# Kernel tuning notes

Measured on AMD Instinct MI355X. Metric: run time of the kernel, lower is better.

The kernel has to match this reference:

```python
import jax, jax.numpy as jnp
import numpy as np

EMBED_DIM = 768
NUM_HEADS = 12
HEAD_DIM = EMBED_DIM // NUM_HEADS  # 64
B, N = 2, 3073
SCALE = HEAD_DIM ** -0.5


def setup_inputs() -> dict:
    key = jax.random.key(0)
    ks = jax.random.split(key, 6)
    s = EMBED_DIM ** -0.5
    return {
        "x": jax.random.normal(ks[0], (B, N, EMBED_DIM), dtype=jnp.float32),
        "qkv_w": jax.random.normal(ks[1], (3 * EMBED_DIM, EMBED_DIM), dtype=jnp.float32) * s,
        "proj_w": jax.random.normal(ks[2], (EMBED_DIM, EMBED_DIM), dtype=jnp.float32) * s,
        "proj_b": jax.random.normal(ks[3], (EMBED_DIM,), dtype=jnp.float32) * 0.02,
        "conv_w": jax.random.normal(ks[4], (HEAD_DIM, 1, 3, 3), dtype=jnp.float32) * 0.02,
        "conv_b": jax.random.normal(ks[5], (HEAD_DIM,), dtype=jnp.float32) * 0.02,
    }


def _local_pos_embed(v, conv_w, conv_b):
    # v: [B, H, N, C] with C = head_dim; drop cls token, fold to spatial grid
    b, h, n, c = v.shape
    u = int(((n - 1) // 12) ** 0.5)
    Hh, Ww = 4 * u, 3 * u
    xs = jnp.transpose(v[:, :, 1:], (0, 1, 3, 2)).reshape(b * h, c, Hh, Ww)
    pe = jax.lax.conv_general_dilated(
        xs, conv_w, window_strides=(1, 1), padding=((1, 1), (1, 1)),
        feature_group_count=c, dimension_numbers=("NCHW", "OIHW", "NCHW"))
    pe = pe + conv_b[None, :, None, None]
    pe = pe.reshape(b, h, c, n - 1).transpose(0, 1, 3, 2)  # [B,H,N-1,C]
    zeros = jnp.zeros((b, h, 1, c), dtype=pe.dtype)
    return jnp.concatenate([zeros, pe], axis=2)  # [B,H,N,C]


def reference(x, qkv_w, proj_w, proj_b, conv_w, conv_b):
    b, n, d = x.shape
    qkv = x @ qkv_w.T  # [B, N, 3D]
    qkv = qkv.reshape(b, n, 3, NUM_HEADS, HEAD_DIM).transpose(2, 0, 3, 1, 4)  # [3,B,H,N,Dh]
    q, k, v = qkv[0], qkv[1], qkv[2]
    scores = jnp.einsum("bhqd,bhkd->bhqk", q, k) * SCALE
    attn = jax.nn.softmax(scores, axis=-1)
    out = jnp.einsum("bham,bhmv->bhav", attn, v)  # [B,H,N,Dh]
    out = out + _local_pos_embed(v, conv_w, conv_b)
    out = out.transpose(0, 2, 1, 3).reshape(b, n, d)  # b h n d -> b n (h d)
    return out @ proj_w.T + proj_b
```

## Files before the change

kernel.cpp:

```cpp
#include <hip/hip_runtime.h>
#include <math.h>

#define NB 2
#define SEQ 3073
#define DIM 768
#define NH 12
#define DH 64
#define HHH 64
#define WWW 48
#define NPATCH 3072
#define QSCALE_L2E 0.18033688f
#define KSPLIT 1536

#define BHN (NB * NH)
#define MROWS (NB * SEQ)
#define MPAD 6272
#define CNT (BHN * SEQ * DH)
#define VTSTRIDE 3136

typedef __attribute__((ext_vector_type(8))) short s8v;
typedef __attribute__((ext_vector_type(4))) float f4v;
typedef __attribute__((ext_vector_type(4))) ushort u4v;

#define MFMA16(a, b, c) __builtin_amdgcn_mfma_f32_16x16x32_bf16((a), (b), (c), 0, 0, 0)

__device__ __forceinline__ ushort f2bf(float f) {
    unsigned x = __float_as_uint(f);
    return (ushort)((x + 0x7FFFu + ((x >> 16) & 1u)) >> 16);
}
__device__ __forceinline__ float bf2f(ushort u) {
    return __uint_as_float(((unsigned)u) << 16);
}
__device__ __forceinline__ unsigned cvt_pk_bf16(float a, float b) {
    unsigned r;
    asm("v_cvt_pk_bf16_f32 %0, %1, %2" : "=v"(r) : "v"(a), "v"(b));
    return r;
}

__device__ __forceinline__ s8v ldsFrag(const ushort* base, int row, int half, int t) {
    int byte = (row * 128 + half * 64 + t * 16) ^ ((row & 7) << 4);
    return *(const s8v*)((const char*)base + byte);
}

__global__ __launch_bounds__(256) void cast_bf16(const float* __restrict__ in,
                                                 ushort* __restrict__ out,
                                                 int n_in, int n_grp) {
    for (int g = blockIdx.x * 256 + threadIdx.x; g < n_grp; g += gridDim.x * 256) {
        int i0 = g * 4;
        float4 vv;
        if (i0 + 4 <= n_in) {
            vv = *(const float4*)(in + i0);
        } else {
            vv.x = (i0 + 0 < n_in) ? in[i0 + 0] : 0.f;
            vv.y = (i0 + 1 < n_in) ? in[i0 + 1] : 0.f;
            vv.z = (i0 + 2 < n_in) ? in[i0 + 2] : 0.f;
            vv.w = (i0 + 3 < n_in) ? in[i0 + 3] : 0.f;
        }
        u4v hv;
        hv[0] = f2bf(vv.x); hv[1] = f2bf(vv.y);
        hv[2] = f2bf(vv.z); hv[3] = f2bf(vv.w);
        *(u4v*)(out + i0) = hv;
    }
}

__global__ __launch_bounds__(256) void split_hilo(const float* __restrict__ in,
                                                  ushort* __restrict__ hi,
                                                  ushort* __restrict__ lo,
                                                  int n_in, int n_grp) {
    for (int g = blockIdx.x * 256 + threadIdx.x; g < n_grp; g += gridDim.x * 256) {
        int i0 = g * 4;
        float4 vv = *(const float4*)(in + i0);
        float v[4] = {vv.x, vv.y, vv.z, vv.w};
        u4v hv, lv;
        #pragma unroll
        for (int j = 0; j < 4; ++j) {
            ushort hb = f2bf(v[j]);
            hv[j] = hb;
            lv[j] = f2bf(v[j] - bf2f(hb));
        }
        *(u4v*)(hi + i0) = hv;
        *(u4v*)(lo + i0) = lv;
    }
}

__device__ __forceinline__ void mfma_tile_768_a1(const ushort* __restrict__ gA,
                                                 const ushort* __restrict__ gBh,
                                                 const ushort* __restrict__ gBl,
                                                 ushort* Ah, ushort* Bh, ushort* Bl,
                                                 f4v acc[4][4]) {
    const int tid = threadIdx.x;
    const int lane = tid & 63;
    const int w = tid >> 6;
    const int lo = lane & 15, t = lane >> 4;
    const int wr = w >> 1, wc = w & 1;

    for (int k0 = 0; k0 < DIM; k0 += 64) {
        __syncthreads();
        #pragma unroll
        for (int i = 0; i < 4; ++i) {
            int s = tid + 256 * i;
            int r = s >> 3, c = s & 7;
            int byte = (r * 128 + c * 16) ^ ((r & 7) << 4);
            size_t go = (size_t)r * DIM + k0 + c * 8;
            s8v a0 = *(const s8v*)(gA + go);
            s8v b0 = *(const s8v*)(gBh + go);
            s8v b1 = *(const s8v*)(gBl + go);
            *(s8v*)((char*)Ah + byte) = a0;
            *(s8v*)((char*)Bh + byte) = b0;
            *(s8v*)((char*)Bl + byte) = b1;
        }
        __syncthreads();

        #pragma unroll
        for (int h = 0; h < 2; ++h) {
            s8v af[4];
            #pragma unroll
            for (int i = 0; i < 4; ++i)
                af[i] = ldsFrag(Ah, wr * 64 + i * 16 + lo, h, t);
            #pragma unroll
            for (int j = 0; j < 4; ++j) {
                int row = wc * 64 + j * 16 + lo;
                s8v bf_h = ldsFrag(Bh, row, h, t);
                s8v bf_l = ldsFrag(Bl, row, h, t);
                #pragma unroll
                for (int i = 0; i < 4; ++i) {
                    acc[i][j] = MFMA16(af[i], bf_h, acc[i][j]);
                    acc[i][j] = MFMA16(af[i], bf_l, acc[i][j]);
                }
            }
        }
    }
}

__global__ __launch_bounds__(256) void qkv_mfma(const ushort* __restrict__ xh,
                                                const ushort* __restrict__ wh,
                                                const ushort* __restrict__ wl,
                                                ushort* __restrict__ q_bf,
                                                ushort* __restrict__ k_bf,
                                                ushort* __restrict__ v_bf,
                                                ushort* __restrict__ vt) {
    __shared__ ushort Ah[8192], Bh[8192], Bl[8192];
    const int m0 = blockIdx.x * 128;
    const int nb = blockIdx.y;
    f4v acc[4][4] = {};
    mfma_tile_768_a1(xh + (size_t)m0 * DIM,
                     wh + (size_t)nb * 128 * DIM, wl + (size_t)nb * 128 * DIM,
                     Ah, Bh, Bl, acc);

    const int tid = threadIdx.x;
    const int lane = tid & 63;
    const int w = tid >> 6;
    const int lo = lane & 15, t = lane >> 4;
    const int wr = w >> 1, wc = w & 1;
    const int which = nb / 6;
    const int rr0 = (nb % 6) * 128;

    #pragma unroll
    for (int i = 0; i < 4; ++i) {
        #pragma unroll
        for (int r = 0; r < 4; ++r) {
            int m = m0 + wr * 64 + i * 16 + t * 4 + r;
            if (m >= MROWS) continue;
            int bb = m / SEQ;
            int row = m - bb * SEQ;
            #pragma unroll
            for (int j = 0; j < 4; ++j) {
                int rr = rr0 + wc * 64 + j * 16 + lo;
                int hh = rr >> 6, dd = rr & 63;
                size_t base = ((size_t)(bb * NH + hh) * SEQ + row) * DH + dd;
                float val = acc[i][j][r];
                if (which == 0) {
                    q_bf[base] = f2bf(val * QSCALE_L2E);
                } else if (which == 1) {
                    k_bf[base] = f2bf(val);
                } else {
                    ushort vb = f2bf(val);
                    v_bf[base] = vb;
                    vt[((size_t)(bb * NH + hh) * DH + dd) * VTSTRIDE + row] = vb;
                }
            }
        }
    }
}

__global__ __launch_bounds__(256) void proj_mfma(const ushort* __restrict__ ah,
                                                 const ushort* __restrict__ pwh,
                                                 const ushort* __restrict__ pwl,
                                                 const float* __restrict__ bias,
                                                 float* __restrict__ out) {
    __shared__ ushort Ah[8192], Bh[8192], Bl[8192];
    const int m0 = blockIdx.x * 128;
    const int nb = blockIdx.y;
    f4v acc[4][4] = {};
    mfma_tile_768_a1(ah + (size_t)m0 * DIM,
                     pwh + (size_t)nb * 128 * DIM, pwl + (size_t)nb * 128 * DIM,
                     Ah, Bh, Bl, acc);

    const int tid = threadIdx.x;
    const int lane = tid & 63;
    const int w = tid >> 6;
    const int lo = lane & 15, t = lane >> 4;
    const int wr = w >> 1, wc = w & 1;

    #pragma unroll
    for (int i = 0; i < 4; ++i) {
        #pragma unroll
        for (int r = 0; r < 4; ++r) {
            int m = m0 + wr * 64 + i * 16 + t * 4 + r;
            if (m >= MROWS) continue;
            #pragma unroll
            for (int j = 0; j < 4; ++j) {
                int n = nb * 128 + wc * 64 + j * 16 + lo;
                out[(size_t)m * DIM + n] = acc[i][j][r] + bias[n];
            }
        }
    }
}

__global__ __launch_bounds__(128, 2) void attn_mfma(const ushort* __restrict__ qh,
                                                    const ushort* __restrict__ kh,
                                                    const ushort* __restrict__ vt,
                                                    float* __restrict__ o0,
                                                    float* __restrict__ o1,
                                                    float* __restrict__ pli) {
    __shared__ __align__(16) ushort Kh[4096];
    __shared__ __align__(16) ushort Vt[5120];
    __shared__ __align__(16) ushort Pl[2][2048];

    const int tid = threadIdx.x;
    const int w = tid >> 6;
    const int lane = tid & 63;
    const int lo = lane & 15;
    const int t = lane >> 4;
    const int bh = blockIdx.y;
    const int q0 = blockIdx.x * 64;
    const int z = blockIdx.z;
    const int kbeg = z * KSPLIT;
    const int kend = z ? SEQ : KSPLIT;

    {
        int rr = 64 + (tid >> 3);
        int col = (tid & 7) * 8;
        int byte = (rr * 128 + col * 2) ^ ((rr & 7) << 4);
        short v = (rr == 64) ? (short)0x3F80 : (short)0;
        s8v ones = {v, v, v, v, v, v, v, v};
        *(s8v*)((char*)Vt + byte) = ones;
    }

    s8v qf0[2], qf1[2];
    #pragma unroll
    for (int g = 0; g < 2; ++g) {
        int qr = q0 + w * 32 + g * 16 + lo;
        if (qr > SEQ - 1) qr = SEQ - 1;
        const size_t qoff = ((size_t)bh * SEQ + qr) * DH + t * 8;
        qf0[g] = *(const s8v*)(qh + qoff);
        qf1[g] = *(const s8v*)(qh + qoff + 32);
    }

    const int rr = tid >> 1;
    const int cc = (tid & 1) * 4;
    int sbyte[4];
    #pragma unroll
    for (int i = 0; i < 4; ++i)
        sbyte[i] = (rr * 128 + (cc + i) * 16) ^ ((rr & 7) << 4);
    const ushort* gk = kh + (size_t)bh * SEQ * DH;
    const ushort* gvb = vt + (size_t)bh * DH * VTSTRIDE;

    s8v pkh[4], pvv[4];
    #pragma unroll
    for (int i = 0; i < 4; ++i) {
        pkh[i] = *(const s8v*)(gk + (size_t)(kbeg + rr) * DH + (cc + i) * 8);
        pvv[i] = *(const s8v*)(gvb + (size_t)rr * VTSTRIDE + kbeg + (cc + i) * 8);
    }

    f4v o[2][5] = {};

    for (int k0 = kbeg; k0 < kend; k0 += 64) {
        #pragma unroll
        for (int i = 0; i < 4; ++i) {
            *(s8v*)((char*)Kh + sbyte[i]) = pkh[i];
            *(s8v*)((char*)Vt + sbyte[i]) = pvv[i];
        }
        __syncthreads();

        const int kn = k0 + 64;
        if (kn < SEQ) {
            #pragma unroll
            for (int i = 0; i < 4; ++i) {
                pkh[i] = *(const s8v*)(gk + (size_t)(kn + rr) * DH + (cc + i) * 8);
                pvv[i] = *(const s8v*)(gvb + (size_t)rr * VTSTRIDE + kn + (cc + i) * 8);
            }
        }

        f4v sv[2][4];
        __builtin_amdgcn_s_setprio(1);
        #pragma unroll
        for (int tc = 0; tc < 4; ++tc) {
            int row = tc * 16 + lo;
            s8v b0 = ldsFrag(Kh, row, 0, t);
            s8v b1 = ldsFrag(Kh, row, 1, t);
            #pragma unroll
            for (int g = 0; g < 2; ++g) {
                f4v a = {0.f, 0.f, 0.f, 0.f};
                a = MFMA16(b0, qf0[g], a);
                a = MFMA16(b1, qf1[g], a);
                sv[g][tc] = a;
            }
        }
        __builtin_amdgcn_s_setprio(0);

        if (k0 + 64 > SEQ) {
            #pragma unroll
            for (int tc = 0; tc < 4; ++tc)
                #pragma unroll
                for (int r = 0; r < 4; ++r)
                    if (k0 + tc * 16 + 4 * t + r >= SEQ) {
                        sv[0][tc][r] = -1e30f;
                        sv[1][tc][r] = -1e30f;
                    }
        }

        #pragma unroll
        for (int g = 0; g < 2; ++g) {
            int prow = g * 16 + lo;
            int rb = prow * 128 + t * 8;
            #pragma unroll
            for (int tc = 0; tc < 4; ++tc) {
                float p0 = exp2f(sv[g][tc][0]);
                float p1 = exp2f(sv[g][tc][1]);
                float p2 = exp2f(sv[g][tc][2]);
                float p3 = exp2f(sv[g][tc][3]);
                uint2 pk;
                pk.x = cvt_pk_bf16(p0, p1);
                pk.y = cvt_pk_bf16(p2, p3);
                int byte = (rb + tc * 32) ^ ((lo & 7) << 4);
                *(uint2*)((char*)Pl[w] + byte) = pk;
            }
        }

        s8v pf0[2], pf1[2];
        #pragma unroll
        for (int g = 0; g < 2; ++g) {
            pf0[g] = ldsFrag(Pl[w], g * 16 + lo, 0, t);
            pf1[g] = ldsFrag(Pl[w], g * 16 + lo, 1, t);
        }
        __builtin_amdgcn_s_setprio(1);
        #pragma unroll
        for (int dt = 0; dt < 5; ++dt) {
            s8v v0 = ldsFrag(Vt, dt * 16 + lo, 0, t);
            s8v v1 = ldsFrag(Vt, dt * 16 + lo, 1, t);
            #pragma unroll
            for (int g = 0; g < 2; ++g) {
                o[g][dt] = MFMA16(pf0[g], v0, o[g][dt]);
                o[g][dt] = MFMA16(pf1[g], v1, o[g][dt]);
            }
        }
        __builtin_amdgcn_s_setprio(0);

        __syncthreads();
    }

    const int b = bh / NH;
    const int h = bh - b * NH;
    float* obase = z ? o1 : o0;
    float* lbase = pli + (size_t)z * BHN * SEQ;
    #pragma unroll
    for (int g = 0; g < 2; ++g) {
        #pragma unroll
        for (int r = 0; r < 4; ++r) {
            int row = q0 + w * 32 + g * 16 + t * 4 + r;
            if (row >= SEQ) continue;
            if (lo == 0)
                lbase[(size_t)bh * SEQ + row] = o[g][4][r];
            #pragma unroll
            for (int dt = 0; dt < 4; ++dt)
                obase[((size_t)(b * SEQ + row)) * DIM + h * DH + dt * 16 + lo] =
                    o[g][dt][r];
        }
    }
}

__global__ __launch_bounds__(256) void conv_pe(const ushort* __restrict__ v,
                                               const float* __restrict__ cw,
                                               const float* __restrict__ cb,
                                               ushort* __restrict__ pe) {
    const int tid = threadIdx.x;
    const int c = tid & 63;
    const int tl = tid >> 6;
    const int blk = blockIdx.x;
    const int bh = blk / 768;
    const int pb = blk - bh * 768;
    const int p = pb * 4 + tl;
    const int y = p / WWW;
    const int x0 = p - y * WWW;

    const ushort* vb = v + (size_t)bh * SEQ * DH;
    float acc = cb[c];
    #pragma unroll
    for (int dy = -1; dy <= 1; ++dy) {
        int yy = y + dy;
        if (yy < 0 || yy >= HHH) continue;
        #pragma unroll
        for (int dx = -1; dx <= 1; ++dx) {
            int xx = x0 + dx;
            if (xx < 0 || xx >= WWW) continue;
            acc = fmaf(bf2f(vb[(size_t)(1 + yy * WWW + xx) * DH + c]),
                       cw[c * 9 + (dy + 1) * 3 + (dx + 1)], acc);
        }
    }
    const int b = bh / NH;
    const int h = bh - b * NH;
    pe[((size_t)(b * SEQ + 1 + p)) * DIM + h * DH + c] = f2bf(acc);
}

__global__ __launch_bounds__(256) void combine_att(const float* __restrict__ o0,
                                                   const float* __restrict__ o1,
                                                   const float* __restrict__ pli,
                                                   const ushort* __restrict__ pe,
                                                   ushort* __restrict__ ah) {
    const int total = MROWS * DIM / 4;
    for (int i = blockIdx.x * 256 + threadIdx.x; i < total; i += gridDim.x * 256) {
        size_t e = (size_t)i * 4;
        int m = (int)(e / DIM);
        int d = (int)(e - (size_t)m * DIM);
        int b = m / SEQ;
        int row = m - b * SEQ;
        int h = d >> 6;
        size_t li = (size_t)(b * NH + h) * SEQ + row;
        float inv = 1.f / (pli[li] + pli[(size_t)BHN * SEQ + li]);
        float4 a = *(const float4*)(o0 + e);
        float4 p = *(const float4*)(o1 + e);
        float pv[4] = {0.f, 0.f, 0.f, 0.f};
        if (row > 0) {
            u4v pb = *(const u4v*)(pe + e);
            #pragma unroll
            for (int j = 0; j < 4; ++j) pv[j] = bf2f(pb[j]);
        }
        u4v rs;
        rs[0] = f2bf(fmaf(a.x + p.x, inv, pv[0]));
        rs[1] = f2bf(fmaf(a.y + p.y, inv, pv[1]));
        rs[2] = f2bf(fmaf(a.z + p.z, inv, pv[2]));
        rs[3] = f2bf(fmaf(a.w + p.w, inv, pv[3]));
        *(u4v*)(ah + e) = rs;
    }
}

extern "C" void kernel_launch(void* const* d_in, const int* in_sizes, int n_in,
                              void* d_out, int out_size, void* d_ws, size_t ws_size,
                              hipStream_t stream) {
    const float* x      = (const float*)d_in[0];
    const float* qkv_w  = (const float*)d_in[1];
    const float* proj_w = (const float*)d_in[2];
    const float* proj_b = (const float*)d_in[3];
    const float* conv_w = (const float*)d_in[4];
    const float* conv_b = (const float*)d_in[5];
    float* out = (float*)d_out;

    ushort* ws = (ushort*)d_ws;
    size_t o = 0;
    ushort* xh  = ws + o; o += (size_t)MPAD * DIM;
    o += (size_t)MPAD * DIM;
    ushort* wh  = ws + o; o += (size_t)2304 * DIM;
    ushort* wl  = ws + o; o += (size_t)2304 * DIM;
    ushort* pwh = ws + o; o += (size_t)DIM * DIM;
    ushort* pwl = ws + o; o += (size_t)DIM * DIM;
    ushort* q_bf = ws + o; o += CNT;
    ushort* k_bf = ws + o; o += CNT;
    ushort* v_bf = ws + o; o += CNT;
    ushort* vtb  = ws + o; o += (size_t)BHN * DH * VTSTRIDE;
    float*  o0   = (float*)(ws + o);
    float*  po1 = (float*)ws;
    float*  pli = (float*)(ws + (size_t)MROWS * DIM * 2);
    ushort* pe  = vtb;
    ushort* ah  = q_bf;

    cast_bf16<<<2048, 256, 0, stream>>>(x, xh, MROWS * DIM, MPAD * DIM / 4);
    split_hilo<<<1024, 256, 0, stream>>>(qkv_w, wh, wl, 2304 * DIM, 2304 * DIM / 4);
    split_hilo<<<512, 256, 0, stream>>>(proj_w, pwh, pwl, DIM * DIM, DIM * DIM / 4);

    qkv_mfma<<<dim3(49, 18), 256, 0, stream>>>(xh, wh, wl, q_bf, k_bf, v_bf, vtb);
    attn_mfma<<<dim3(49, BHN, 2), 128, 0, stream>>>(q_bf, k_bf, vtb, o0, po1, pli);
    conv_pe<<<BHN * (NPATCH / 4), 256, 0, stream>>>(v_bf, conv_w, conv_b, pe);
    combine_att<<<2048, 256, 0, stream>>>(o0, po1, pli, pe, ah);
    proj_mfma<<<dim3(49, 6), 256, 0, stream>>>(ah, pwh, pwl, proj_b, out);
}
```

Before: 269.9 us.

## Load attention K/V fragments directly from global memory and remap blocks per XCD

The attention kernel no longer stages K and V tiles through shared memory with barriers. Each wave now loads its MFMA fragments straight from global memory, relying on L2 for reuse. The row-sum is computed in registers from the exponentials plus shuffles instead of an extra ones-column MFMA tile. Blocks are launched on a flat grid remapped so each of the 8 XCDs works on contiguous head groups for L2 locality. The cost is redundant global and L2 traffic per wave and exposed load latency without a prefetch pipeline.

After: 390.7 us. +44.7%, slower.

```diff
diff --git a/kernel.cpp b/kernel.cpp
--- a/kernel.cpp
+++ b/kernel.cpp
@@ -217,14 +217,12 @@
     }
 }
 
-__global__ __launch_bounds__(128, 2) void attn_mfma(const ushort* __restrict__ qh,
-                                                    const ushort* __restrict__ kh,
-                                                    const ushort* __restrict__ vt,
-                                                    float* __restrict__ o0,
-                                                    float* __restrict__ o1,
-                                                    float* __restrict__ pli) {
-    __shared__ __align__(16) ushort Kh[4096];
-    __shared__ __align__(16) ushort Vt[5120];
+__global__ __launch_bounds__(128) void attn_mfma(const ushort* __restrict__ qh,
+                                                 const ushort* __restrict__ kh,
+                                                 const ushort* __restrict__ vt,
+                                                 float* __restrict__ o0,
+                                                 float* __restrict__ o1,
+                                                 float* __restrict__ pli) {
     __shared__ __align__(16) ushort Pl[2][2048];
 
     const int tid = threadIdx.x;
@@ -232,20 +230,16 @@
     const int lane = tid & 63;
     const int lo = lane & 15;
     const int t = lane >> 4;
-    const int bh = blockIdx.y;
-    const int q0 = blockIdx.x * 64;
-    const int z = blockIdx.z;
+
+    const int flat = blockIdx.x;
+    const int work = (flat & 7) * 294 + (flat >> 3);
+    const int bh = work / 98;
+    const int rem = work - bh * 98;
+    const int z = rem / 49;
+    const int qb = rem - z * 49;
+    const int q0 = qb * 64;
     const int kbeg = z * KSPLIT;
     const int kend = z ? SEQ : KSPLIT;
-
-    {
-        int rr = 64 + (tid >> 3);
-        int col = (tid & 7) * 8;
-        int byte = (rr * 128 + col * 2) ^ ((rr & 7) << 4);
-        short v = (rr == 64) ? (short)0x3F80 : (short)0;
-        s8v ones = {v, v, v, v, v, v, v, v};
-        *(s8v*)((char*)Vt + byte) = ones;
-    }
 
     s8v qf0[2], qf1[2];
     #pragma unroll
@@ -257,48 +251,20 @@
         qf1[g] = *(const s8v*)(qh + qoff + 32);
     }
 
-    const int rr = tid >> 1;
-    const int cc = (tid & 1) * 4;
-    int sbyte[4];
-    #pragma unroll
-    for (int i = 0; i < 4; ++i)
-        sbyte[i] = (rr * 128 + (cc + i) * 16) ^ ((rr & 7) << 4);
-    const ushort* gk = kh + (size_t)bh * SEQ * DH;
-    const ushort* gvb = vt + (size_t)bh * DH * VTSTRIDE;
-
-    s8v pkh[4], pvv[4];
-    #pragma unroll
-    for (int i = 0; i < 4; ++i) {
-        pkh[i] = *(const s8v*)(gk + (size_t)(kbeg + rr) * DH + (cc + i) * 8);
-        pvv[i] = *(const s8v*)(gvb + (size_t)rr * VTSTRIDE + kbeg + (cc + i) * 8);
-    }
-
-    f4v o[2][5] = {};
+    const ushort* gk  = kh + (size_t)bh * SEQ * DH + t * 8;
+    const ushort* gvb = vt + (size_t)bh * DH * VTSTRIDE + t * 8;
+
+    f4v o[2][4] = {};
+    float lp[2] = {0.f, 0.f};
 
     for (int k0 = kbeg; k0 < kend; k0 += 64) {
-        #pragma unroll
-        for (int i = 0; i < 4; ++i) {
-            *(s8v*)((char*)Kh + sbyte[i]) = pkh[i];
-            *(s8v*)((char*)Vt + sbyte[i]) = pvv[i];
-        }
-        __syncthreads();
-
-        const int kn = k0 + 64;
-        if (kn < SEQ) {
-            #pragma unroll
-            for (int i = 0; i < 4; ++i) {
-                pkh[i] = *(const s8v*)(gk + (size_t)(kn + rr) * DH + (cc + i) * 8);
-                pvv[i] = *(const s8v*)(gvb + (size_t)rr * VTSTRIDE + kn + (cc + i) * 8);
-            }
-        }
-
         f4v sv[2][4];
         __builtin_amdgcn_s_setprio(1);
         #pragma unroll
         for (int tc = 0; tc < 4; ++tc) {
-            int row = tc * 16 + lo;
-            s8v b0 = ldsFrag(Kh, row, 0, t);
-            s8v b1 = ldsFrag(Kh, row, 1, t);
+            const ushort* kr = gk + (size_t)(k0 + tc * 16 + lo) * DH;
+            s8v b0 = *(const s8v*)(kr);
+            s8v b1 = *(const s8v*)(kr + 32);
             #pragma unroll
             for (int g = 0; g < 2; ++g) {
                 f4v a = {0.f, 0.f, 0.f, 0.f};
@@ -330,6 +296,7 @@
                 float p1 = exp2f(sv[g][tc][1]);
                 float p2 = exp2f(sv[g][tc][2]);
                 float p3 = exp2f(sv[g][tc][3]);
+                lp[g] += (p0 + p1) + (p2 + p3);
                 uint2 pk;
                 pk.x = cvt_pk_bf16(p0, p1);
                 pk.y = cvt_pk_bf16(p2, p3);
@@ -346,9 +313,10 @@
         }
         __builtin_amdgcn_s_setprio(1);
         #pragma unroll
-        for (int dt = 0; dt < 5; ++dt) {
-            s8v v0 = ldsFrag(Vt, dt * 16 + lo, 0, t);
-            s8v v1 = ldsFrag(Vt, dt * 16 + lo, 1, t);
+        for (int dt = 0; dt < 4; ++dt) {
+            const ushort* vr = gvb + (size_t)(dt * 16 + lo) * VTSTRIDE + k0;
+            s8v v0 = *(const s8v*)(vr);
+            s8v v1 = *(const s8v*)(vr + 32);
             #pragma unroll
             for (int g = 0; g < 2; ++g) {
                 o[g][dt] = MFMA16(pf0[g], v0, o[g][dt]);
@@ -356,8 +324,12 @@
             }
         }
         __builtin_amdgcn_s_setprio(0);
-
-        __syncthreads();
+    }
+
+    #pragma unroll
+    for (int g = 0; g < 2; ++g) {
+        lp[g] += __shfl_xor(lp[g], 16);
+        lp[g] += __shfl_xor(lp[g], 32);
     }
 
     const int b = bh / NH;
@@ -366,12 +338,15 @@
     float* lbase = pli + (size_t)z * BHN * SEQ;
     #pragma unroll
     for (int g = 0; g < 2; ++g) {
+        if (t == 0) {
+            int row = q0 + w * 32 + g * 16 + lo;
+            if (row < SEQ)
+                lbase[(size_t)bh * SEQ + row] = lp[g];
+        }
         #pragma unroll
         for (int r = 0; r < 4; ++r) {
             int row = q0 + w * 32 + g * 16 + t * 4 + r;
             if (row >= SEQ) continue;
-            if (lo == 0)
-                lbase[(size_t)bh * SEQ + row] = o[g][4][r];
             #pragma unroll
             for (int dt = 0; dt < 4; ++dt)
                 obase[((size_t)(b * SEQ + row)) * DIM + h * DH + dt * 16 + lo] =
@@ -479,7 +454,7 @@
     split_hilo<<<512, 256, 0, stream>>>(proj_w, pwh, pwl, DIM * DIM, DIM * DIM / 4);
 
     qkv_mfma<<<dim3(49, 18), 256, 0, stream>>>(xh, wh, wl, q_bf, k_bf, v_bf, vtb);
-    attn_mfma<<<dim3(49, BHN, 2), 128, 0, stream>>>(q_bf, k_bf, vtb, o0, po1, pli);
+    attn_mfma<<<2352, 128, 0, stream>>>(q_bf, k_bf, vtb, o0, po1, pli);
     conv_pe<<<BHN * (NPATCH / 4), 256, 0, stream>>>(v_bf, conv_w, conv_b, pe);
     combine_att<<<2048, 256, 0, stream>>>(o0, po1, pli, pe, ah);
     proj_mfma<<<dim3(49, 6), 256, 0, stream>>>(ah, pwh, pwl, proj_b, out);
```
